# Kernel optimization log

Measured on AMD Instinct MI355X. Metric: run time of the kernel, lower is better.

## Reference

```python
import jax, jax.numpy as jnp
import numpy as np

FEATURE_DIM = 256
NUM_HEADS = 8
HEAD_DIM = FEATURE_DIM // NUM_HEADS
LOCAL_RADIUS = 3.0
N_CUR = 4096
N_HIST = 4096
COORD_EXTENT = 16.0


def setup_inputs() -> dict:
    key = jax.random.key(0)
    ks = jax.random.split(key, 12)
    s = 1.0 / np.sqrt(FEATURE_DIM)  # ~nn.Linear init scale
    return {
        "current_feats": jax.random.normal(ks[0], (N_CUR, FEATURE_DIM), jnp.float32),
        "historical_feats": jax.random.normal(ks[1], (N_HIST, FEATURE_DIM), jnp.float32),
        "current_coords": jax.random.uniform(ks[2], (N_CUR, 3), jnp.float32) * COORD_EXTENT,
        "historical_coords": jax.random.uniform(ks[3], (N_HIST, 3), jnp.float32) * COORD_EXTENT,
        "Wq": jax.random.normal(ks[4], (FEATURE_DIM, FEATURE_DIM), jnp.float32) * s,
        "bq": jnp.zeros((FEATURE_DIM,), jnp.float32),
        "Wk": jax.random.normal(ks[5], (FEATURE_DIM, FEATURE_DIM), jnp.float32) * s,
        "bk": jnp.zeros((FEATURE_DIM,), jnp.float32),
        "Wv": jax.random.normal(ks[6], (FEATURE_DIM, FEATURE_DIM), jnp.float32) * s,
        "bv": jnp.zeros((FEATURE_DIM,), jnp.float32),
        "Wo": jax.random.normal(ks[7], (FEATURE_DIM, FEATURE_DIM), jnp.float32) * s,
        "bo": jnp.zeros((FEATURE_DIM,), jnp.float32),
    }


def reference(current_feats, historical_feats, current_coords, historical_coords,
              Wq, bq, Wk, bk, Wv, bv, Wo, bo):
    # local mask: squared distance <= radius^2 (identical to norm <= radius)
    diff = current_coords[:, None, :] - historical_coords[None, :, :]  # [Nq, Nk, 3]
    local_mask = jnp.sum(diff * diff, axis=-1) <= LOCAL_RADIUS ** 2      # [Nq, Nk]

    q = (current_feats @ Wq.T + bq).reshape(N_CUR, NUM_HEADS, HEAD_DIM)
    k = (historical_feats @ Wk.T + bk).reshape(N_HIST, NUM_HEADS, HEAD_DIM)
    v = (historical_feats @ Wv.T + bv).reshape(N_HIST, NUM_HEADS, HEAD_DIM)

    scores = jnp.einsum('qhd,khd->qhk', q, k) / np.sqrt(HEAD_DIM)        # [Nq, H, Nk]
    scores = jnp.where(local_mask[:, None, :], scores, -jnp.inf)
    attn = jax.nn.softmax(scores, axis=-1)  # dropout is identity in eval
    out = jnp.einsum('qhk,khd->qhd', attn, v).reshape(N_CUR, FEATURE_DIM)
    return out @ Wo.T + bo
```

## Files before the change

kernel.cpp:

```cpp
#include <hip/hip_runtime.h>
#include <math.h>

#define FDIM 256
#define NH 8
#define HD 32
#define NQ 4096
#define NKEY 4096
#define CAP 512
#define R2 9.0f

typedef _Float16 half8 __attribute__((ext_vector_type(8)));
typedef _Float16 half4v __attribute__((ext_vector_type(4)));
typedef float f32x4 __attribute__((ext_vector_type(4)));
typedef unsigned short ushort_t;

#define CB_CUR  0
#define CB_HIST 1048576
#define CB_WQ   2097152
#define CB_WK   2162688
#define CB_WV   2228224
#define CB_WO   2293760
#define CB_F4_TOTAL 589824

__global__ __launch_bounds__(256) void prep(const float* __restrict__ cur,
                                            const float* __restrict__ hist,
                                            const float* __restrict__ Wq,
                                            const float* __restrict__ Wk,
                                            const float* __restrict__ Wv,
                                            const float* __restrict__ Wo,
                                            _Float16* __restrict__ dst,
                                            const float* __restrict__ qc,
                                            const float* __restrict__ kc,
                                            ushort_t* __restrict__ nbr,
                                            int* __restrict__ cnt) {
    if (blockIdx.x < 1024) {
        const int q    = blockIdx.x * 4 + (threadIdx.x >> 6);
        const int lane = threadIdx.x & 63;
        const float qx = qc[q * 3 + 0];
        const float qy = qc[q * 3 + 1];
        const float qz = qc[q * 3 + 2];
        int base = 0;
        for (int k0 = 0; k0 < NKEY; k0 += 64) {
            const int k = k0 + lane;
            float dx = __fsub_rn(qx, kc[k * 3 + 0]);
            float dy = __fsub_rn(qy, kc[k * 3 + 1]);
            float dz = __fsub_rn(qz, kc[k * 3 + 2]);
            float d2 = __fadd_rn(__fadd_rn(__fmul_rn(dx, dx), __fmul_rn(dy, dy)),
                                 __fmul_rn(dz, dz));
            bool valid = (d2 <= R2);
            unsigned long long bal = __ballot(valid);
            if (valid) {
                int pos = base + __popcll(bal & ((1ull << lane) - 1ull));
                if (pos < CAP) nbr[(size_t)q * CAP + pos] = (ushort_t)k;
            }
            base += __popcll(bal);
        }
        if (lane == 0) cnt[q] = (base > CAP) ? CAP : base;
    } else {
        const int stride = 1024 * 256;
        for (int i4 = (blockIdx.x - 1024) * 256 + threadIdx.x; i4 < CB_F4_TOTAL;
             i4 += stride) {
            const float* src;
            int base;
            if (i4 < 262144)      { src = cur;  base = 0; }
            else if (i4 < 524288) { src = hist; base = 262144; }
            else if (i4 < 540672) { src = Wq;   base = 524288; }
            else if (i4 < 557056) { src = Wk;   base = 540672; }
            else if (i4 < 573440) { src = Wv;   base = 557056; }
            else                  { src = Wo;   base = 573440; }
            float4 v = ((const float4*)src)[i4 - base];
            half4v h;
            h[0] = (_Float16)v.x; h[1] = (_Float16)v.y;
            h[2] = (_Float16)v.z; h[3] = (_Float16)v.w;
            ((half4v*)dst)[i4] = h;
        }
    }
}

__device__ __forceinline__ void mfma_tile_16x64(const _Float16* __restrict__ A,
                                                const _Float16* __restrict__ W,
                                                int m0, int n0, int wave, int lane,
                                                f32x4 acc[4]) {
    const int row  = lane & 15;
    const int quad = lane >> 4;
    const _Float16* aptr = A + (size_t)(m0 + wave * 16 + row) * 256 + quad * 8;
    const _Float16* wptr = W + (size_t)(n0 + row) * 256 + quad * 8;
#pragma unroll
    for (int i = 0; i < 4; ++i) acc[i] = (f32x4){0.f, 0.f, 0.f, 0.f};
#pragma unroll
    for (int k0 = 0; k0 < 8; ++k0) {
        half8 a = *(const half8*)(aptr + k0 * 32);
#pragma unroll
        for (int nt = 0; nt < 4; ++nt) {
            half8 b = *(const half8*)(wptr + (size_t)nt * 16 * 256 + k0 * 32);
            acc[nt] = __builtin_amdgcn_mfma_f32_16x16x32_f16(a, b, acc[nt], 0, 0, 0);
        }
    }
}

__global__ __launch_bounds__(256) void qkv_mfma(const _Float16* __restrict__ cb,
                                                const float* __restrict__ bq,
                                                const float* __restrict__ bk,
                                                const float* __restrict__ bv,
                                                _Float16* __restrict__ Qh,
                                                _Float16* __restrict__ KV) {
    const int z    = blockIdx.z;
    const int wave = threadIdx.x >> 6;
    const int lane = threadIdx.x & 63;
    const int m0   = blockIdx.y * 64;
    const int n0   = blockIdx.x * 64;

    const _Float16* A = (z == 0) ? (cb + CB_CUR) : (cb + CB_HIST);
    const _Float16* W = (z == 0) ? (cb + CB_WQ) : (z == 1) ? (cb + CB_WK) : (cb + CB_WV);
    const float* bias = (z == 0) ? bq : (z == 1) ? bk : bv;

    f32x4 acc[4];
    mfma_tile_16x64(A, W, m0, n0, wave, lane, acc);

    const int col  = lane & 15;
    const int quad = lane >> 4;
    float bs[4];
#pragma unroll
    for (int nt = 0; nt < 4; ++nt) bs[nt] = bias[n0 + nt * 16 + col];

    if (z == 0) {
#pragma unroll
        for (int nt = 0; nt < 4; ++nt)
#pragma unroll
            for (int r = 0; r < 4; ++r)
                Qh[(size_t)(m0 + wave * 16 + quad * 4 + r) * 256 + n0 + nt * 16 + col] =
                    (_Float16)(acc[nt][r] + bs[nt]);
    } else {
        const int off = (z == 1) ? 0 : 256;
#pragma unroll
        for (int nt = 0; nt < 4; ++nt)
#pragma unroll
            for (int r = 0; r < 4; ++r)
                KV[(size_t)(m0 + wave * 16 + quad * 4 + r) * 512 + off + n0 + nt * 16 + col] =
                    (_Float16)(acc[nt][r] + bs[nt]);
    }
}

__global__ __launch_bounds__(256) void o_mfma(const _Float16* __restrict__ Ob,
                                              const _Float16* __restrict__ Wo,
                                              const float* __restrict__ bo,
                                              float* __restrict__ out) {
    const int wave = threadIdx.x >> 6;
    const int lane = threadIdx.x & 63;
    const int m0   = blockIdx.y * 64;
    const int n0   = blockIdx.x * 64;

    f32x4 acc[4];
    mfma_tile_16x64(Ob, Wo, m0, n0, wave, lane, acc);

    const int col  = lane & 15;
    const int quad = lane >> 4;
#pragma unroll
    for (int nt = 0; nt < 4; ++nt) {
        const float b = bo[n0 + nt * 16 + col];
#pragma unroll
        for (int r = 0; r < 4; ++r)
            out[(size_t)(m0 + wave * 16 + quad * 4 + r) * 256 + n0 + nt * 16 + col] =
                acc[nt][r] + b;
    }
}

__global__ __launch_bounds__(256) void sparse_attn9(const _Float16* __restrict__ Qh,
                                                    const _Float16* __restrict__ KV,
                                                    const ushort_t* __restrict__ nbr,
                                                    const int* __restrict__ cnt,
                                                    _Float16* __restrict__ Ob) {
    __shared__ float sm[4][32][12];
    const int q    = blockIdx.x;
    const int t    = threadIdx.x;
    const int wave = t >> 6;
    const int lane = t & 63;
    const int p    = lane >> 5;
    const int h    = (lane >> 2) & 7;
    const int s    = lane & 3;

    float qv[8];
    {
        half8 qh = *(const half8*)(Qh + (size_t)q * FDIM + h * HD + s * 8);
        const float sc = 0.17677669529663687f;
#pragma unroll
        for (int i = 0; i < 8; ++i) qv[i] = (float)qh[i] * sc;
    }

    float o[8];
#pragma unroll
    for (int i = 0; i < 8; ++i) o[i] = 0.f;
    float l = 0.f;

    const int n = cnt[q];
    const ushort_t* nl = nbr + (size_t)q * CAP;
    const int koff = h * HD + s * 8;

    for (int j = 2 * wave + p; j < n; j += 8) {
        const int k = nl[j];
        const _Float16* r = KV + ((size_t)k << 9) + koff;
        half8 k8 = *(const half8*)(r);
        half8 v8 = *(const half8*)(r + 256);

        float part = 0.f;
#pragma unroll
        for (int i = 0; i < 8; ++i)
            part = fmaf(qv[i], (float)k8[i], part);
        part += __shfl_xor(part, 1, 64);
        part += __shfl_xor(part, 2, 64);

        const float pw = __expf(part);
        l += pw;
#pragma unroll
        for (int i = 0; i < 8; ++i)
            o[i] = fmaf(pw, (float)v8[i], o[i]);
    }

    l += __shfl_xor(l, 32, 64);
#pragma unroll
    for (int i = 0; i < 8; ++i) o[i] += __shfl_xor(o[i], 32, 64);

    if (lane < 32) {
        float* dst = &sm[wave][lane][0];
        *(float4*)(dst)     = (float4){o[0], o[1], o[2], o[3]};
        *(float4*)(dst + 4) = (float4){o[4], o[5], o[6], o[7]};
        dst[8] = l;
    }
    __syncthreads();

    if (t < 32) {
        float4 x0 = *(const float4*)&sm[0][t][0];
        float4 x1 = *(const float4*)&sm[0][t][4];
        float O[8] = {x0.x, x0.y, x0.z, x0.w, x1.x, x1.y, x1.z, x1.w};
        float L = sm[0][t][8];
#pragma unroll
        for (int w = 1; w < 4; ++w) {
            float4 y0 = *(const float4*)&sm[w][t][0];
            float4 y1 = *(const float4*)&sm[w][t][4];
            L += sm[w][t][8];
            O[0] += y0.x; O[1] += y0.y; O[2] += y0.z; O[3] += y0.w;
            O[4] += y1.x; O[5] += y1.y; O[6] += y1.z; O[7] += y1.w;
        }
        const float inv = 1.0f / L;
        half8 ho;
#pragma unroll
        for (int i = 0; i < 8; ++i) ho[i] = (_Float16)(O[i] * inv);
        *(half8*)(Ob + (size_t)q * FDIM + t * 8) = ho;
    }
}

extern "C" void kernel_launch(void* const* d_in, const int* in_sizes, int n_in,
                              void* d_out, int out_size, void* d_ws, size_t ws_size,
                              hipStream_t stream) {
    const float* cur_feats   = (const float*)d_in[0];
    const float* hist_feats  = (const float*)d_in[1];
    const float* cur_coords  = (const float*)d_in[2];
    const float* hist_coords = (const float*)d_in[3];
    const float* bq = (const float*)d_in[5];
    const float* bk = (const float*)d_in[7];
    const float* bv = (const float*)d_in[9];
    const float* bo = (const float*)d_in[11];
    float* out = (float*)d_out;

    char* w = (char*)d_ws;
    _Float16*  Qh   = (_Float16*)(w);
    _Float16*  KV   = (_Float16*)(w + (4 << 20));
    ushort_t*  nbr  = (ushort_t*)(w + (8 << 20));
    int*       cnt  = (int*)(w + (12 << 20));
    _Float16*  Ob   = (_Float16*)(w + (12 << 20) + (64 << 10));
    _Float16*  cb   = (_Float16*)(w + (15 << 20));

    prep<<<2048, 256, 0, stream>>>(cur_feats, hist_feats,
                                   (const float*)d_in[4], (const float*)d_in[6],
                                   (const float*)d_in[8], (const float*)d_in[10], cb,
                                   cur_coords, hist_coords, nbr, cnt);

    qkv_mfma<<<dim3(4, 64, 3), 256, 0, stream>>>(cb, bq, bk, bv, Qh, KV);

    sparse_attn9<<<NQ, 256, 0, stream>>>(Qh, KV, nbr, cnt, Ob);

    o_mfma<<<dim3(4, 64), 256, 0, stream>>>(Ob, cb + CB_WO, bo, out);
}
```

Measured before the change: 145.9 us.

## Pair spatially close queries per block and share K/V loads over neighbor union

Queries are bucketed into a 6x6x6 spatial grid during prep, with an overflow list for full cells. The attention kernel then processes two queries from the same cell per block. It merges their sorted neighbor lists into a union in shared memory so each K/V row is fetched once and applied to both queries under per-query masks. The aim is to cut redundant gather traffic, at the cost of list merging with binary searches, shared-memory atomics, extra syncs, and a memset and extra prep blocks.

```diff
diff --git a/kernel.cpp b/kernel.cpp
--- a/kernel.cpp
+++ b/kernel.cpp
@@ -8,6 +8,13 @@
 #define NKEY 4096
 #define CAP 512
 #define R2 9.0f
+
+#define NCELL 6
+#define NC3   216
+#define CCAP  64
+#define GBLK  (NC3 * 32)
+#define OCAP  512
+#define OBLK  32
 
 typedef _Float16 half8 __attribute__((ext_vector_type(8)));
 typedef _Float16 half4v __attribute__((ext_vector_type(4)));
@@ -32,7 +39,11 @@
                                             const float* __restrict__ qc,
                                             const float* __restrict__ kc,
                                             ushort_t* __restrict__ nbr,
-                                            int* __restrict__ cnt) {
+                                            int* __restrict__ cnt,
+                                            int* __restrict__ ccnt,
+                                            int* __restrict__ cellq,
+                                            int* __restrict__ ocnt,
+                                            int* __restrict__ oq) {
     if (blockIdx.x < 1024) {
         const int q    = blockIdx.x * 4 + (threadIdx.x >> 6);
         const int lane = threadIdx.x & 63;
@@ -56,7 +67,7 @@
             base += __popcll(bal);
         }
         if (lane == 0) cnt[q] = (base > CAP) ? CAP : base;
-    } else {
+    } else if (blockIdx.x < 2048) {
         const int stride = 1024 * 256;
         for (int i4 = (blockIdx.x - 1024) * 256 + threadIdx.x; i4 < CB_F4_TOTAL;
              i4 += stride) {
@@ -74,6 +85,19 @@
             h[2] = (_Float16)v.z; h[3] = (_Float16)v.w;
             ((half4v*)dst)[i4] = h;
         }
+    } else {
+        const int q = (blockIdx.x - 2048) * 256 + threadIdx.x;
+        const float s = (float)NCELL / 16.0f;
+        int ix = (int)(qc[q * 3 + 0] * s);
+        int iy = (int)(qc[q * 3 + 1] * s);
+        int iz = (int)(qc[q * 3 + 2] * s);
+        ix = min(NCELL - 1, max(0, ix));
+        iy = min(NCELL - 1, max(0, iy));
+        iz = min(NCELL - 1, max(0, iz));
+        const int cell = (iz * NCELL + iy) * NCELL + ix;
+        const int slot = atomicAdd(&ccnt[cell], 1);
+        if (slot < CCAP) cellq[cell * CCAP + slot] = q;
+        else { int o = atomicAdd(ocnt, 1); if (o < OCAP) oq[o] = q; }
     }
 }
 
@@ -165,87 +189,167 @@
     }
 }
 
-__global__ __launch_bounds__(256) void sparse_attn9(const _Float16* __restrict__ Qh,
-                                                    const _Float16* __restrict__ KV,
-                                                    const ushort_t* __restrict__ nbr,
-                                                    const int* __restrict__ cnt,
-                                                    _Float16* __restrict__ Ob) {
-    __shared__ float sm[4][32][12];
-    const int q    = blockIdx.x;
+__device__ __forceinline__ int lb16(const ushort_t* a, int n, int key) {
+    int lo = 0, hi = n;
+    while (lo < hi) { int mid = (lo + hi) >> 1; if (a[mid] < key) lo = mid + 1; else hi = mid; }
+    return lo;
+}
+
+__device__ __forceinline__ void process_pair(
+        int q0, int q1, int nq,
+        const _Float16* __restrict__ Qh, const _Float16* __restrict__ KV,
+        const ushort_t* __restrict__ nbr, const int* __restrict__ cnt,
+        _Float16* __restrict__ Ob,
+        ushort_t* sl0, ushort_t* sl1, unsigned int* ulist, int* ucnt,
+        float (*sm)[32][18]) {
     const int t    = threadIdx.x;
     const int wave = t >> 6;
     const int lane = t & 63;
     const int p    = lane >> 5;
-    const int h    = (lane >> 2) & 7;
-    const int s    = lane & 3;
-
-    float qv[8];
+    const int hs   = lane & 31;
+
+    const int n0 = cnt[q0];
+    const int n1 = (nq == 2) ? cnt[q1] : 0;
+
+    for (int i = t; i < n0; i += 256) sl0[i] = nbr[(size_t)q0 * CAP + i];
+    for (int i = t; i < n1; i += 256) sl1[i] = nbr[(size_t)q1 * CAP + i];
+    if (t == 0) *ucnt = 0;
+    __syncthreads();
+
+    for (int i = t; i < n0; i += 256) {
+        const int key = sl0[i];
+        const int j   = lb16(sl1, n1, key);
+        const int f1  = (j < n1 && sl1[j] == key) ? 1 : 0;
+        ulist[atomicAdd(ucnt, 1)] = (unsigned int)key | (1u << 16) | ((unsigned int)f1 << 17);
+    }
+    for (int i = t; i < n1; i += 256) {
+        const int key = sl1[i];
+        const int j   = lb16(sl0, n0, key);
+        if (!(j < n0 && sl0[j] == key))
+            ulist[atomicAdd(ucnt, 1)] = (unsigned int)key | (2u << 16);
+    }
+    __syncthreads();
+    const int U = *ucnt;
+
+    float qv0[8], qv1[8];
     {
-        half8 qh = *(const half8*)(Qh + (size_t)q * FDIM + h * HD + s * 8);
         const float sc = 0.17677669529663687f;
-#pragma unroll
-        for (int i = 0; i < 8; ++i) qv[i] = (float)qh[i] * sc;
-    }
-
-    float o[8];
-#pragma unroll
-    for (int i = 0; i < 8; ++i) o[i] = 0.f;
-    float l = 0.f;
-
-    const int n = cnt[q];
-    const ushort_t* nl = nbr + (size_t)q * CAP;
-    const int koff = h * HD + s * 8;
-
-    for (int j = 2 * wave + p; j < n; j += 8) {
-        const int k = nl[j];
+        half8 a = *(const half8*)(Qh + (size_t)q0 * FDIM + hs * 8);
+        half8 b = *(const half8*)(Qh + (size_t)q1 * FDIM + hs * 8);
+#pragma unroll
+        for (int i = 0; i < 8; ++i) { qv0[i] = (float)a[i] * sc; qv1[i] = (float)b[i] * sc; }
+    }
+
+    float o0[8], o1[8];
+#pragma unroll
+    for (int i = 0; i < 8; ++i) { o0[i] = 0.f; o1[i] = 0.f; }
+    float l0 = 0.f, l1 = 0.f;
+
+    const int koff = hs * 8;
+    for (int j = 2 * wave + p; j < U; j += 8) {
+        const unsigned int e = ulist[j];
+        const int k = e & 0xFFFF;
         const _Float16* r = KV + ((size_t)k << 9) + koff;
         half8 k8 = *(const half8*)(r);
         half8 v8 = *(const half8*)(r + 256);
 
-        float part = 0.f;
-#pragma unroll
-        for (int i = 0; i < 8; ++i)
-            part = fmaf(qv[i], (float)k8[i], part);
-        part += __shfl_xor(part, 1, 64);
-        part += __shfl_xor(part, 2, 64);
-
-        const float pw = __expf(part);
-        l += pw;
-#pragma unroll
-        for (int i = 0; i < 8; ++i)
-            o[i] = fmaf(pw, (float)v8[i], o[i]);
-    }
-
-    l += __shfl_xor(l, 32, 64);
-#pragma unroll
-    for (int i = 0; i < 8; ++i) o[i] += __shfl_xor(o[i], 32, 64);
+        float d0 = 0.f, d1 = 0.f;
+#pragma unroll
+        for (int i = 0; i < 8; ++i) {
+            const float kf = (float)k8[i];
+            d0 = fmaf(qv0[i], kf, d0);
+            d1 = fmaf(qv1[i], kf, d1);
+        }
+        d0 += __shfl_xor(d0, 1, 64); d0 += __shfl_xor(d0, 2, 64);
+        d1 += __shfl_xor(d1, 1, 64); d1 += __shfl_xor(d1, 2, 64);
+
+        const float pw0 = (e & (1u << 16)) ? __expf(d0) : 0.f;
+        const float pw1 = (e & (1u << 17)) ? __expf(d1) : 0.f;
+        l0 += pw0; l1 += pw1;
+#pragma unroll
+        for (int i = 0; i < 8; ++i) {
+            const float vf = (float)v8[i];
+            o0[i] = fmaf(pw0, vf, o0[i]);
+            o1[i] = fmaf(pw1, vf, o1[i]);
+        }
+    }
+
+    l0 += __shfl_xor(l0, 32, 64);
+    l1 += __shfl_xor(l1, 32, 64);
+#pragma unroll
+    for (int i = 0; i < 8; ++i) {
+        o0[i] += __shfl_xor(o0[i], 32, 64);
+        o1[i] += __shfl_xor(o1[i], 32, 64);
+    }
 
     if (lane < 32) {
-        float* dst = &sm[wave][lane][0];
-        *(float4*)(dst)     = (float4){o[0], o[1], o[2], o[3]};
-        *(float4*)(dst + 4) = (float4){o[4], o[5], o[6], o[7]};
-        dst[8] = l;
+        float* d = &sm[wave][lane][0];
+        *(float4*)(d)      = (float4){o0[0], o0[1], o0[2], o0[3]};
+        *(float4*)(d + 4)  = (float4){o0[4], o0[5], o0[6], o0[7]};
+        d[8] = l0;
+        *(float4*)(d + 9)  = (float4){o1[0], o1[1], o1[2], o1[3]};
+        *(float4*)(d + 13) = (float4){o1[4], o1[5], o1[6], o1[7]};
+        d[17] = l1;
     }
     __syncthreads();
 
     if (t < 32) {
-        float4 x0 = *(const float4*)&sm[0][t][0];
-        float4 x1 = *(const float4*)&sm[0][t][4];
-        float O[8] = {x0.x, x0.y, x0.z, x0.w, x1.x, x1.y, x1.z, x1.w};
-        float L = sm[0][t][8];
+        float O0[8], O1[8], L0, L1;
+        {
+            const float* d = &sm[0][t][0];
+#pragma unroll
+            for (int i = 0; i < 8; ++i) { O0[i] = d[i]; O1[i] = d[9 + i]; }
+            L0 = d[8]; L1 = d[17];
+        }
 #pragma unroll
         for (int w = 1; w < 4; ++w) {
-            float4 y0 = *(const float4*)&sm[w][t][0];
-            float4 y1 = *(const float4*)&sm[w][t][4];
-            L += sm[w][t][8];
-            O[0] += y0.x; O[1] += y0.y; O[2] += y0.z; O[3] += y0.w;
-            O[4] += y1.x; O[5] += y1.y; O[6] += y1.z; O[7] += y1.w;
-        }
-        const float inv = 1.0f / L;
-        half8 ho;
-#pragma unroll
-        for (int i = 0; i < 8; ++i) ho[i] = (_Float16)(O[i] * inv);
-        *(half8*)(Ob + (size_t)q * FDIM + t * 8) = ho;
+            const float* d = &sm[w][t][0];
+#pragma unroll
+            for (int i = 0; i < 8; ++i) { O0[i] += d[i]; O1[i] += d[9 + i]; }
+            L0 += d[8]; L1 += d[17];
+        }
+        const float inv0 = 1.0f / L0;
+        half8 h0;
+#pragma unroll
+        for (int i = 0; i < 8; ++i) h0[i] = (_Float16)(O0[i] * inv0);
+        *(half8*)(Ob + (size_t)q0 * FDIM + t * 8) = h0;
+        if (nq == 2) {
+            const float inv1 = 1.0f / L1;
+            half8 h1;
+#pragma unroll
+            for (int i = 0; i < 8; ++i) h1[i] = (_Float16)(O1[i] * inv1);
+            *(half8*)(Ob + (size_t)q1 * FDIM + t * 8) = h1;
+        }
+    }
+    __syncthreads();
+}
+
+__global__ __launch_bounds__(256) void sparse_attn10(
+        const _Float16* __restrict__ Qh, const _Float16* __restrict__ KV,
+        const ushort_t* __restrict__ nbr, const int* __restrict__ cnt,
+        const int* __restrict__ ccnt, const int* __restrict__ cellq,
+        const int* __restrict__ ocnt, const int* __restrict__ oq,
+        _Float16* __restrict__ Ob) {
+    __shared__ ushort_t sl0[CAP], sl1[CAP];
+    __shared__ unsigned int ulist[2 * CAP];
+    __shared__ int ucnt;
+    __shared__ float sm[4][32][18];
+
+    if (blockIdx.x < GBLK) {
+        const int c  = blockIdx.x >> 5;
+        const int i  = blockIdx.x & 31;
+        const int cc = min(ccnt[c], CCAP);
+        if (2 * i >= cc) return;
+        const int q0 = cellq[c * CCAP + 2 * i];
+        const int nq = (2 * i + 1 < cc) ? 2 : 1;
+        const int q1 = (nq == 2) ? cellq[c * CCAP + 2 * i + 1] : q0;
+        process_pair(q0, q1, nq, Qh, KV, nbr, cnt, Ob, sl0, sl1, ulist, &ucnt, sm);
+    } else {
+        const int oc = min(*ocnt, OCAP);
+        for (int i = blockIdx.x - GBLK; i < oc; i += OBLK) {
+            const int qq = oq[i];
+            process_pair(qq, qq, 1, Qh, KV, nbr, cnt, Ob, sl0, sl1, ulist, &ucnt, sm);
+        }
     }
 }
 
@@ -269,15 +373,23 @@
     int*       cnt  = (int*)(w + (12 << 20));
     _Float16*  Ob   = (_Float16*)(w + (12 << 20) + (64 << 10));
     _Float16*  cb   = (_Float16*)(w + (15 << 20));
-
-    prep<<<2048, 256, 0, stream>>>(cur_feats, hist_feats,
+    int*       ccnt = (int*)(w + (20 << 20));
+    int*       ocnt = ccnt + NC3;
+    int*       cellq= (int*)(w + (20 << 20) + 1024);
+    int*       oq   = (int*)(w + (20 << 20) + 1024 + NC3 * CCAP * 4);
+
+    hipMemsetAsync(ccnt, 0, (NC3 + 1) * sizeof(int), stream);
+
+    prep<<<2064, 256, 0, stream>>>(cur_feats, hist_feats,
                                    (const float*)d_in[4], (const float*)d_in[6],
                                    (const float*)d_in[8], (const float*)d_in[10], cb,
-                                   cur_coords, hist_coords, nbr, cnt);
+                                   cur_coords, hist_coords, nbr, cnt,
+                                   ccnt, cellq, ocnt, oq);
 
     qkv_mfma<<<dim3(4, 64, 3), 256, 0, stream>>>(cb, bq, bk, bv, Qh, KV);
 
-    sparse_attn9<<<NQ, 256, 0, stream>>>(Qh, KV, nbr, cnt, Ob);
+    sparse_attn10<<<GBLK + OBLK, 256, 0, stream>>>(Qh, KV, nbr, cnt,
+                                                   ccnt, cellq, ocnt, oq, Ob);
 
     o_mfma<<<dim3(4, 64), 256, 0, stream>>>(Ob, cb + CB_WO, bo, out);
 }
```

Result: slower. 187.4 us (+28.5%).

## Fuse feature fp16 conversion into QKV GEMM and process two queries per attention block

Applied to the files above, without the earlier changes.

The prep kernel no longer converts the current and historical feature matrices to fp16. The QKV MFMA kernel now reads fp32 features directly and converts them in registers, which removes a full write and reread of 4 MB of fp16 features. The attention kernel is also restructured so each block handles two queries with a grid of 2048, amortizing per-block setup at the cost of an extra barrier. The A-operand loads in the GEMM become twice as wide in bytes, and the features are re-read and re-converted once per output-column tile.

```diff
diff --git a/kernel.cpp b/kernel.cpp
--- a/kernel.cpp
+++ b/kernel.cpp
@@ -14,25 +14,21 @@
 typedef float f32x4 __attribute__((ext_vector_type(4)));
 typedef unsigned short ushort_t;
 
-#define CB_CUR  0
-#define CB_HIST 1048576
-#define CB_WQ   2097152
-#define CB_WK   2162688
-#define CB_WV   2228224
-#define CB_WO   2293760
-#define CB_F4_TOTAL 589824
-
-__global__ __launch_bounds__(256) void prep(const float* __restrict__ cur,
-                                            const float* __restrict__ hist,
-                                            const float* __restrict__ Wq,
-                                            const float* __restrict__ Wk,
-                                            const float* __restrict__ Wv,
-                                            const float* __restrict__ Wo,
-                                            _Float16* __restrict__ dst,
-                                            const float* __restrict__ qc,
-                                            const float* __restrict__ kc,
-                                            ushort_t* __restrict__ nbr,
-                                            int* __restrict__ cnt) {
+#define CBW_WQ 0
+#define CBW_WK 65536
+#define CBW_WV 131072
+#define CBW_WO 196608
+#define CBW_F4 65536
+
+__global__ __launch_bounds__(256) void prep2(const float* __restrict__ Wq,
+                                             const float* __restrict__ Wk,
+                                             const float* __restrict__ Wv,
+                                             const float* __restrict__ Wo,
+                                             _Float16* __restrict__ cbw,
+                                             const float* __restrict__ qc,
+                                             const float* __restrict__ kc,
+                                             ushort_t* __restrict__ nbr,
+                                             int* __restrict__ cnt) {
     if (blockIdx.x < 1024) {
         const int q    = blockIdx.x * 4 + (threadIdx.x >> 6);
         const int lane = threadIdx.x & 63;
@@ -57,22 +53,47 @@
         }
         if (lane == 0) cnt[q] = (base > CAP) ? CAP : base;
     } else {
-        const int stride = 1024 * 256;
-        for (int i4 = (blockIdx.x - 1024) * 256 + threadIdx.x; i4 < CB_F4_TOTAL;
+        const int stride = 64 * 256;
+        for (int i4 = (blockIdx.x - 1024) * 256 + threadIdx.x; i4 < CBW_F4;
              i4 += stride) {
             const float* src;
             int base;
-            if (i4 < 262144)      { src = cur;  base = 0; }
-            else if (i4 < 524288) { src = hist; base = 262144; }
-            else if (i4 < 540672) { src = Wq;   base = 524288; }
-            else if (i4 < 557056) { src = Wk;   base = 540672; }
-            else if (i4 < 573440) { src = Wv;   base = 557056; }
-            else                  { src = Wo;   base = 573440; }
+            if (i4 < 16384)      { src = Wq; base = 0; }
+            else if (i4 < 32768) { src = Wk; base = 16384; }
+            else if (i4 < 49152) { src = Wv; base = 32768; }
+            else                 { src = Wo; base = 49152; }
             float4 v = ((const float4*)src)[i4 - base];
             half4v h;
             h[0] = (_Float16)v.x; h[1] = (_Float16)v.y;
             h[2] = (_Float16)v.z; h[3] = (_Float16)v.w;
-            ((half4v*)dst)[i4] = h;
+            ((half4v*)cbw)[i4] = h;
+        }
+    }
+}
+
+__device__ __forceinline__ void mfma_tile_16x64_af32(const float* __restrict__ A,
+                                                     const _Float16* __restrict__ W,
+                                                     int m0, int n0, int wave, int lane,
+                                                     f32x4 acc[4]) {
+    const int row  = lane & 15;
+    const int quad = lane >> 4;
+    const float*    aptr = A + (size_t)(m0 + wave * 16 + row) * 256 + quad * 8;
+    const _Float16* wptr = W + (size_t)(n0 + row) * 256 + quad * 8;
+#pragma unroll
+    for (int i = 0; i < 4; ++i) acc[i] = (f32x4){0.f, 0.f, 0.f, 0.f};
+#pragma unroll
+    for (int k0 = 0; k0 < 8; ++k0) {
+        float4 a0 = *(const float4*)(aptr + k0 * 32);
+        float4 a1 = *(const float4*)(aptr + k0 * 32 + 4);
+        half8 a;
+        a[0] = (_Float16)a0.x; a[1] = (_Float16)a0.y;
+        a[2] = (_Float16)a0.z; a[3] = (_Float16)a0.w;
+        a[4] = (_Float16)a1.x; a[5] = (_Float16)a1.y;
+        a[6] = (_Float16)a1.z; a[7] = (_Float16)a1.w;
+#pragma unroll
+        for (int nt = 0; nt < 4; ++nt) {
+            half8 b = *(const half8*)(wptr + (size_t)nt * 16 * 256 + k0 * 32);
+            acc[nt] = __builtin_amdgcn_mfma_f32_16x16x32_f16(a, b, acc[nt], 0, 0, 0);
         }
     }
 }
@@ -98,24 +119,26 @@
     }
 }
 
-__global__ __launch_bounds__(256) void qkv_mfma(const _Float16* __restrict__ cb,
-                                                const float* __restrict__ bq,
-                                                const float* __restrict__ bk,
-                                                const float* __restrict__ bv,
-                                                _Float16* __restrict__ Qh,
-                                                _Float16* __restrict__ KV) {
+__global__ __launch_bounds__(256) void qkv_mfma2(const float* __restrict__ cur,
+                                                 const float* __restrict__ hist,
+                                                 const _Float16* __restrict__ cbw,
+                                                 const float* __restrict__ bq,
+                                                 const float* __restrict__ bk,
+                                                 const float* __restrict__ bv,
+                                                 _Float16* __restrict__ Qh,
+                                                 _Float16* __restrict__ KV) {
     const int z    = blockIdx.z;
     const int wave = threadIdx.x >> 6;
     const int lane = threadIdx.x & 63;
     const int m0   = blockIdx.y * 64;
     const int n0   = blockIdx.x * 64;
 
-    const _Float16* A = (z == 0) ? (cb + CB_CUR) : (cb + CB_HIST);
-    const _Float16* W = (z == 0) ? (cb + CB_WQ) : (z == 1) ? (cb + CB_WK) : (cb + CB_WV);
+    const float* A = (z == 0) ? cur : hist;
+    const _Float16* W = cbw + ((z == 0) ? CBW_WQ : (z == 1) ? CBW_WK : CBW_WV);
     const float* bias = (z == 0) ? bq : (z == 1) ? bk : bv;
 
     f32x4 acc[4];
-    mfma_tile_16x64(A, W, m0, n0, wave, lane, acc);
+    mfma_tile_16x64_af32(A, W, m0, n0, wave, lane, acc);
 
     const int col  = lane & 15;
     const int quad = lane >> 4;
@@ -165,87 +188,91 @@
     }
 }
 
-__global__ __launch_bounds__(256) void sparse_attn9(const _Float16* __restrict__ Qh,
-                                                    const _Float16* __restrict__ KV,
-                                                    const ushort_t* __restrict__ nbr,
-                                                    const int* __restrict__ cnt,
-                                                    _Float16* __restrict__ Ob) {
+__global__ __launch_bounds__(256) void sparse_attn12(const _Float16* __restrict__ Qh,
+                                                     const _Float16* __restrict__ KV,
+                                                     const ushort_t* __restrict__ nbr,
+                                                     const int* __restrict__ cnt,
+                                                     _Float16* __restrict__ Ob) {
     __shared__ float sm[4][32][12];
-    const int q    = blockIdx.x;
     const int t    = threadIdx.x;
     const int wave = t >> 6;
     const int lane = t & 63;
     const int p    = lane >> 5;
     const int h    = (lane >> 2) & 7;
     const int s    = lane & 3;
-
-    float qv[8];
-    {
-        half8 qh = *(const half8*)(Qh + (size_t)q * FDIM + h * HD + s * 8);
-        const float sc = 0.17677669529663687f;
-#pragma unroll
-        for (int i = 0; i < 8; ++i) qv[i] = (float)qh[i] * sc;
-    }
-
-    float o[8];
-#pragma unroll
-    for (int i = 0; i < 8; ++i) o[i] = 0.f;
-    float l = 0.f;
-
-    const int n = cnt[q];
-    const ushort_t* nl = nbr + (size_t)q * CAP;
     const int koff = h * HD + s * 8;
 
-    for (int j = 2 * wave + p; j < n; j += 8) {
-        const int k = nl[j];
-        const _Float16* r = KV + ((size_t)k << 9) + koff;
-        half8 k8 = *(const half8*)(r);
-        half8 v8 = *(const half8*)(r + 256);
-
-        float part = 0.f;
-#pragma unroll
-        for (int i = 0; i < 8; ++i)
-            part = fmaf(qv[i], (float)k8[i], part);
-        part += __shfl_xor(part, 1, 64);
-        part += __shfl_xor(part, 2, 64);
-
-        const float pw = __expf(part);
-        l += pw;
-#pragma unroll
-        for (int i = 0; i < 8; ++i)
-            o[i] = fmaf(pw, (float)v8[i], o[i]);
-    }
-
-    l += __shfl_xor(l, 32, 64);
-#pragma unroll
-    for (int i = 0; i < 8; ++i) o[i] += __shfl_xor(o[i], 32, 64);
-
-    if (lane < 32) {
-        float* dst = &sm[wave][lane][0];
-        *(float4*)(dst)     = (float4){o[0], o[1], o[2], o[3]};
-        *(float4*)(dst + 4) = (float4){o[4], o[5], o[6], o[7]};
-        dst[8] = l;
-    }
-    __syncthreads();
-
-    if (t < 32) {
-        float4 x0 = *(const float4*)&sm[0][t][0];
-        float4 x1 = *(const float4*)&sm[0][t][4];
-        float O[8] = {x0.x, x0.y, x0.z, x0.w, x1.x, x1.y, x1.z, x1.w};
-        float L = sm[0][t][8];
-#pragma unroll
-        for (int w = 1; w < 4; ++w) {
-            float4 y0 = *(const float4*)&sm[w][t][0];
-            float4 y1 = *(const float4*)&sm[w][t][4];
-            L += sm[w][t][8];
-            O[0] += y0.x; O[1] += y0.y; O[2] += y0.z; O[3] += y0.w;
-            O[4] += y1.x; O[5] += y1.y; O[6] += y1.z; O[7] += y1.w;
-        }
-        const float inv = 1.0f / L;
-        half8 ho;
-#pragma unroll
-        for (int i = 0; i < 8; ++i) ho[i] = (_Float16)(O[i] * inv);
-        *(half8*)(Ob + (size_t)q * FDIM + t * 8) = ho;
+    for (int qi = 0; qi < 2; ++qi) {
+        const int q = blockIdx.x + qi * 2048;
+
+        float qv[8];
+        {
+            half8 qh = *(const half8*)(Qh + (size_t)q * FDIM + koff);
+            const float sc = 0.17677669529663687f;
+#pragma unroll
+            for (int i = 0; i < 8; ++i) qv[i] = (float)qh[i] * sc;
+        }
+
+        float o[8];
+#pragma unroll
+        for (int i = 0; i < 8; ++i) o[i] = 0.f;
+        float l = 0.f;
+
+        const int n = cnt[q];
+        const ushort_t* nl = nbr + (size_t)q * CAP;
+
+        for (int j = 2 * wave + p; j < n; j += 8) {
+            const int k = nl[j];
+            const _Float16* r = KV + ((size_t)k << 9) + koff;
+            half8 k8 = *(const half8*)(r);
+            half8 v8 = *(const half8*)(r + 256);
+
+            float part = 0.f;
+#pragma unroll
+            for (int i = 0; i < 8; ++i)
+                part = fmaf(qv[i], (float)k8[i], part);
+            part += __shfl_xor(part, 1, 64);
+            part += __shfl_xor(part, 2, 64);
+
+            const float pw = __expf(part);
+            l += pw;
+#pragma unroll
+            for (int i = 0; i < 8; ++i)
+                o[i] = fmaf(pw, (float)v8[i], o[i]);
+        }
+
+        l += __shfl_xor(l, 32, 64);
+#pragma unroll
+        for (int i = 0; i < 8; ++i) o[i] += __shfl_xor(o[i], 32, 64);
+
+        if (lane < 32) {
+            float* dst = &sm[wave][lane][0];
+            *(float4*)(dst)     = (float4){o[0], o[1], o[2], o[3]};
+            *(float4*)(dst + 4) = (float4){o[4], o[5], o[6], o[7]};
+            dst[8] = l;
+        }
+        __syncthreads();
+
+        if (t < 32) {
+            float4 x0 = *(const float4*)&sm[0][t][0];
+            float4 x1 = *(const float4*)&sm[0][t][4];
+            float O[8] = {x0.x, x0.y, x0.z, x0.w, x1.x, x1.y, x1.z, x1.w};
+            float L = sm[0][t][8];
+#pragma unroll
+            for (int w = 1; w < 4; ++w) {
+                float4 y0 = *(const float4*)&sm[w][t][0];
+                float4 y1 = *(const float4*)&sm[w][t][4];
+                L += sm[w][t][8];
+                O[0] += y0.x; O[1] += y0.y; O[2] += y0.z; O[3] += y0.w;
+                O[4] += y1.x; O[5] += y1.y; O[6] += y1.z; O[7] += y1.w;
+            }
+            const float inv = 1.0f / L;
+            half8 ho;
+#pragma unroll
+            for (int i = 0; i < 8; ++i) ho[i] = (_Float16)(O[i] * inv);
+            *(half8*)(Ob + (size_t)q * FDIM + t * 8) = ho;
+        }
+        __syncthreads();
     }
 }
 
@@ -256,9 +283,13 @@
     const float* hist_feats  = (const float*)d_in[1];
     const float* cur_coords  = (const float*)d_in[2];
     const float* hist_coords = (const float*)d_in[3];
+    const float* Wq = (const float*)d_in[4];
     const float* bq = (const float*)d_in[5];
+    const float* Wk = (const float*)d_in[6];
     const float* bk = (const float*)d_in[7];
+    const float* Wv = (const float*)d_in[8];
     const float* bv = (const float*)d_in[9];
+    const float* Wo = (const float*)d_in[10];
     const float* bo = (const float*)d_in[11];
     float* out = (float*)d_out;
 
@@ -268,16 +299,15 @@
     ushort_t*  nbr  = (ushort_t*)(w + (8 << 20));
     int*       cnt  = (int*)(w + (12 << 20));
     _Float16*  Ob   = (_Float16*)(w + (12 << 20) + (64 << 10));
-    _Float16*  cb   = (_Float16*)(w + (15 << 20));
-
-    prep<<<2048, 256, 0, stream>>>(cur_feats, hist_feats,
-                                   (const float*)d_in[4], (const float*)d_in[6],
-                                   (const float*)d_in[8], (const float*)d_in[10], cb,
-                                   cur_coords, hist_coords, nbr, cnt);
-
-    qkv_mfma<<<dim3(4, 64, 3), 256, 0, stream>>>(cb, bq, bk, bv, Qh, KV);
-
-    sparse_attn9<<<NQ, 256, 0, stream>>>(Qh, KV, nbr, cnt, Ob);
-
-    o_mfma<<<dim3(4, 64), 256, 0, stream>>>(Ob, cb + CB_WO, bo, out);
-}
+    _Float16*  cbw  = (_Float16*)(w + (15 << 20));
+
+    prep2<<<1088, 256, 0, stream>>>(Wq, Wk, Wv, Wo, cbw,
+                                    cur_coords, hist_coords, nbr, cnt);
+
+    qkv_mfma2<<<dim3(4, 64, 3), 256, 0, stream>>>(cur_feats, hist_feats, cbw,
+                                                  bq, bk, bv, Qh, KV);
+
+    sparse_attn12<<<2048, 256, 0, stream>>>(Qh, KV, nbr, cnt, Ob);
+
+    o_mfma<<<dim3(4, 64), 256, 0, stream>>>(Ob, cbw + CBW_WO, bo, out);
+}
```

Result: no change. 148.0 us (+1.5%).
